# Optimization experiments

Hardware: AMD Instinct MI355X
Metric: run time of the kernel (lower is better)

The kernel has to match this reference:

```python
import jax, jax.numpy as jnp
import numpy as np

N_NODES = 100000
EPS = 1e-12  # F.normalize eps


def mean_aggregate(x, src, dst):
    # gather source features along edges, segment-mean into destinations
    msg = x[src]                                              # [E, D]
    summed = jax.ops.segment_sum(msg, dst, num_segments=N_NODES)  # [N, D]
    cnt = jax.ops.segment_sum(jnp.ones_like(dst, dtype=x.dtype), dst,
                              num_segments=N_NODES)           # [N]
    return summed / jnp.maximum(cnt, 1.0)[:, None]


def sage_conv(x, src, dst, W_l, b_l, W_r, normalize):
    agg = mean_aggregate(x, src, dst)
    out = agg @ W_l.T + b_l + x @ W_r.T  # lin_l(mean neigh) + lin_r(root)
    if normalize:
        norm = jnp.sqrt(jnp.sum(out * out, axis=-1, keepdims=True))
        out = out / jnp.maximum(norm, EPS)
    return out


def setup_inputs() -> dict:
    key = jax.random.key(0)
    ks = jax.random.split(key, 8)
    H, O = 128, 128
    s = 1.0 / np.sqrt(H)
    x = jax.random.normal(ks[0], (N_NODES, H), dtype=jnp.float32)
    edge_index = jax.random.randint(ks[1], (2, 1600000), 0, N_NODES, dtype=jnp.int64)
    return {
        "x": x,
        "edge_index": edge_index,
        "W1l": jax.random.uniform(ks[2], (H, H), jnp.float32, -s, s),
        "b1": jax.random.uniform(ks[3], (H,), jnp.float32, -s, s),
        "W1r": jax.random.uniform(ks[4], (H, H), jnp.float32, -s, s),
        "W2l": jax.random.uniform(ks[5], (O, H), jnp.float32, -s, s),
        "b2": jax.random.uniform(ks[6], (O,), jnp.float32, -s, s),
        "W2r": jax.random.uniform(ks[7], (O, H), jnp.float32, -s, s),
    }


def reference(x, edge_index, W1l, b1, W1r, W2l, b2, W2r):
    src, dst = edge_index[0], edge_index[1]
    h = sage_conv(x, src, dst, W1l, b1, W1r, normalize=True)
    h = jax.nn.relu(h)
    out = sage_conv(h, src, dst, W2l, b2, W2r, normalize=False)
    return out
```

## Files before the change

kernel.cpp:

```cpp
#include <hip/hip_runtime.h>
#include <hip/hip_bf16.h>
#include <hip/hip_fp16.h>

#define N_NODES 100000
#define DFEAT 128
#define SLAB 4096
#define BSHIFT 9
#define NBUCK 196

#define WS_CNT      0
#define WS_W16      100000
#define WS_BCNT     180000
#define WS_BBASE    180200
#define WS_BCUR     180400
#define WS_OFFS     200000
#define WS_ESRC     300608
#define WS_AGGH     1900608
#define WS_CASTH    8300608

typedef _Float16 half8 __attribute__((ext_vector_type(8)));
typedef _Float16 half2v __attribute__((ext_vector_type(2)));
typedef float floatx4 __attribute__((ext_vector_type(4)));

__global__ __launch_bounds__(256) void cast_x_kernel(const float* __restrict__ x,
                                                     __half* __restrict__ xh, int total4) {
    int stride = gridDim.x * 256;
    for (int i = blockIdx.x * 256 + threadIdx.x; i < total4; i += stride) {
        float4 v = ((const float4*)x)[i];
        __half2 h01 = __floats2half2_rn(v.x, v.y);
        __half2 h23 = __floats2half2_rn(v.z, v.w);
        uint2 o;
        o.x = *(unsigned int*)&h01;
        o.y = *(unsigned int*)&h23;
        ((uint2*)xh)[i] = o;
    }
}

__global__ __launch_bounds__(256) void cast_w_kernel(const float* __restrict__ W1l,
                                                     const float* __restrict__ W1r,
                                                     const float* __restrict__ W2l,
                                                     const float* __restrict__ W2r,
                                                     __half* __restrict__ w16) {
    int i = blockIdx.x * 256 + threadIdx.x;
    int m = i >> 12;
    int off = i & 4095;
    const float* Wp = (m == 0) ? W1l : (m == 1) ? W1r : (m == 2) ? W2l : W2r;
    float4 v = ((const float4*)Wp)[off];
    __half2 h01 = __floats2half2_rn(v.x, v.y);
    __half2 h23 = __floats2half2_rn(v.z, v.w);
    uint2 o;
    o.x = *(unsigned int*)&h01;
    o.y = *(unsigned int*)&h23;
    ((uint2*)w16)[i] = o;
}

__global__ __launch_bounds__(1024) void hist_kernel(const int* __restrict__ dst,
                                                    int* __restrict__ bcnt, int E) {
    __shared__ int lh[NBUCK];
    int t = threadIdx.x;
    if (t < NBUCK) lh[t] = 0;
    __syncthreads();
    int s0 = blockIdx.x * SLAB, s1 = min(E, s0 + SLAB);
    for (int i = s0 + t; i < s1; i += 1024)
        atomicAdd(&lh[dst[i] >> BSHIFT], 1);
    __syncthreads();
    if (t < NBUCK && lh[t] > 0) atomicAdd(&bcnt[t], lh[t]);
}

__global__ void bscan_kernel(const int* __restrict__ bcnt, int* __restrict__ bbase,
                             int* __restrict__ bcur, int E) {
    __shared__ int s[256];
    int t = threadIdx.x;
    int v = (t < NBUCK) ? bcnt[t] : 0;
    s[t] = v;
    __syncthreads();
    for (int d = 1; d < 256; d <<= 1) {
        int u = (t >= d) ? s[t - d] : 0;
        __syncthreads();
        s[t] += u;
        __syncthreads();
    }
    if (t < NBUCK) {
        int excl = s[t] - v;
        bbase[t] = excl;
        bcur[t] = excl;
    }
    if (t == 0) bbase[NBUCK] = E;
}

__global__ __launch_bounds__(512) void phase2_kernel(const int* __restrict__ src,
                                                     const int* __restrict__ dst,
                                                     int* __restrict__ bcur,
                                                     int* __restrict__ pairs,
                                                     int E) {
    __shared__ int lbase[NBUCK];
    __shared__ int lcur[NBUCK];
    __shared__ int lgb[NBUCK];
    __shared__ int sc[256];
    __shared__ int2 lp[SLAB];
    int b = blockIdx.x;
    int t = threadIdx.x;
    if (t < NBUCK) lbase[t] = 0;
    __syncthreads();
    int s0 = b * SLAB, s1 = min(E, s0 + SLAB);
    for (int i = s0 + t; i < s1; i += 512)
        atomicAdd(&lbase[dst[i] >> BSHIFT], 1);
    __syncthreads();
    int v = (t < NBUCK) ? lbase[t] : 0;
    if (t < 256) sc[t] = v;
    __syncthreads();
    for (int d = 1; d < 256; d <<= 1) {
        int u = (t >= d && t < 256) ? sc[t - d] : 0;
        __syncthreads();
        if (t < 256) sc[t] += u;
        __syncthreads();
    }
    if (t < NBUCK) {
        int excl = sc[t] - v;
        lbase[t] = excl;
        lcur[t] = excl;
        lgb[t] = (v > 0) ? atomicAdd(&bcur[t], v) : 0;
    }
    __syncthreads();
    for (int i = s0 + t; i < s1; i += 512) {
        int d = dst[i];
        int s = src[i];
        int bk = d >> BSHIFT;
        int pos = atomicAdd(&lcur[bk], 1);
        lp[pos] = make_int2(s, d);
    }
    __syncthreads();
    int m = s1 - s0;
    for (int i = t; i < m; i += 512) {
        int2 p = lp[i];
        int bk = p.y >> BSHIFT;
        pairs[lgb[bk] + (i - lbase[bk])] = ((p.y & 511) << 17) | p.x;
    }
}

__global__ __launch_bounds__(1024) void phase3_kernel(const int* __restrict__ pairs,
                                                      const int* __restrict__ bbase,
                                                      int* __restrict__ cnt,
                                                      int* __restrict__ offs,
                                                      int* __restrict__ esrc,
                                                      int n) {
    __shared__ int lcnt[512];
    __shared__ int sc[512];
    __shared__ int lexcl[512];
    int g = blockIdx.x;
    int node0 = g << BSHIFT;
    int t = threadIdx.x;
    if (t < 512) lcnt[t] = 0;
    __syncthreads();
    int S = bbase[g];
    int Eg = bbase[g + 1];
    for (int i = S + t; i < Eg; i += 1024)
        atomicAdd(&lcnt[pairs[i] >> 17], 1);
    __syncthreads();
    int v = (t < 512) ? lcnt[t] : 0;
    if (t < 512) sc[t] = v;
    __syncthreads();
    for (int d = 1; d < 512; d <<= 1) {
        int u = (t >= d && t < 512) ? sc[t - d] : 0;
        __syncthreads();
        if (t < 512) sc[t] += u;
        __syncthreads();
    }
    if (t < 512) {
        int excl = sc[t] - v;
        lexcl[t] = excl;
        int nd = node0 + t;
        if (nd < n) {
            cnt[nd] = v;
            offs[nd] = S + excl;
        }
    }
    __syncthreads();
    for (int i = S + t; i < Eg; i += 1024) {
        int p = pairs[i];
        int pos = atomicAdd(&lexcl[p >> 17], 1);
        esrc[S + pos] = p & 0x1FFFF;
    }
}

#define ACC(c, r)                        \
    s[c][0] += *(half2v*)&(r).x;         \
    s[c][1] += *(half2v*)&(r).y;         \
    s[c][2] += *(half2v*)&(r).z;         \
    s[c][3] += *(half2v*)&(r).w;

__global__ void aggregate_kernel(const __half* __restrict__ feat, const int* __restrict__ esrc,
                                 const int* __restrict__ offs, const int* __restrict__ cnt,
                                 __half* __restrict__ agg, int n) {
    int wid = (blockIdx.x * blockDim.x + threadIdx.x) >> 6;
    int lane = threadIdx.x & 63;
    int grp = lane >> 4;
    int l15 = lane & 15;
    int node = wid * 4 + grp;
    if (node >= n) return;
    int beg = offs[node];
    int deg = cnt[node];
    const _Float16* fbase = (const _Float16*)feat + l15 * 8;
    const int* ep = esrc + beg;

    half2v s[4][4];
#pragma unroll
    for (int c = 0; c < 4; c++)
#pragma unroll
        for (int k = 0; k < 4; k++) s[c][k] = (half2v)(_Float16)0;

    int j = 0;
    for (; j + 8 <= deg; j += 8) {
        int i0 = ep[j + 0], i1 = ep[j + 1], i2 = ep[j + 2], i3 = ep[j + 3];
        int i4 = ep[j + 4], i5 = ep[j + 5], i6 = ep[j + 6], i7 = ep[j + 7];
        uint4 r0 = *(const uint4*)(fbase + (size_t)i0 * DFEAT);
        uint4 r1 = *(const uint4*)(fbase + (size_t)i1 * DFEAT);
        uint4 r2 = *(const uint4*)(fbase + (size_t)i2 * DFEAT);
        uint4 r3 = *(const uint4*)(fbase + (size_t)i3 * DFEAT);
        uint4 r4 = *(const uint4*)(fbase + (size_t)i4 * DFEAT);
        uint4 r5 = *(const uint4*)(fbase + (size_t)i5 * DFEAT);
        uint4 r6 = *(const uint4*)(fbase + (size_t)i6 * DFEAT);
        uint4 r7 = *(const uint4*)(fbase + (size_t)i7 * DFEAT);
        ACC(0, r0) ACC(1, r1) ACC(2, r2) ACC(3, r3)
        ACC(0, r4) ACC(1, r5) ACC(2, r6) ACC(3, r7)
    }
    for (; j + 4 <= deg; j += 4) {
        int i0 = ep[j + 0], i1 = ep[j + 1], i2 = ep[j + 2], i3 = ep[j + 3];
        uint4 r0 = *(const uint4*)(fbase + (size_t)i0 * DFEAT);
        uint4 r1 = *(const uint4*)(fbase + (size_t)i1 * DFEAT);
        uint4 r2 = *(const uint4*)(fbase + (size_t)i2 * DFEAT);
        uint4 r3 = *(const uint4*)(fbase + (size_t)i3 * DFEAT);
        ACC(0, r0) ACC(1, r1) ACC(2, r2) ACC(3, r3)
    }
    if (j < deg) {
        int rem = deg - j;
        int i0 = ep[j];
        int i1 = ep[j + (rem > 1 ? 1 : 0)];
        int i2 = ep[j + (rem > 2 ? 2 : 0)];
        uint4 r0 = *(const uint4*)(fbase + (size_t)i0 * DFEAT);
        uint4 r1 = *(const uint4*)(fbase + (size_t)i1 * DFEAT);
        uint4 r2 = *(const uint4*)(fbase + (size_t)i2 * DFEAT);
        if (rem < 2) { r1.x = 0u; r1.y = 0u; r1.z = 0u; r1.w = 0u; }
        if (rem < 3) { r2.x = 0u; r2.y = 0u; r2.z = 0u; r2.w = 0u; }
        ACC(0, r0) ACC(1, r1) ACC(2, r2)
    }

    float scale = 1.0f / fmaxf((float)deg, 1.0f);
    float a[8];
#pragma unroll
    for (int k = 0; k < 4; k++) {
        a[2 * k]     = ((float)s[0][k].x + (float)s[1][k].x) + ((float)s[2][k].x + (float)s[3][k].x);
        a[2 * k + 1] = ((float)s[0][k].y + (float)s[1][k].y) + ((float)s[2][k].y + (float)s[3][k].y);
    }
    __half2 h0 = __floats2half2_rn(a[0] * scale, a[1] * scale);
    __half2 h1 = __floats2half2_rn(a[2] * scale, a[3] * scale);
    __half2 h2 = __floats2half2_rn(a[4] * scale, a[5] * scale);
    __half2 h3 = __floats2half2_rn(a[6] * scale, a[7] * scale);
    uint4 o;
    o.x = *(unsigned int*)&h0;
    o.y = *(unsigned int*)&h1;
    o.z = *(unsigned int*)&h2;
    o.w = *(unsigned int*)&h3;
    *(uint4*)(agg + (size_t)node * DFEAT + l15 * 8) = o;
}

template <bool NORM_RELU>
__global__ __launch_bounds__(256) void gemm64_kernel(
    const __half* __restrict__ A1_, const __half* __restrict__ A2_,
    const __half* __restrict__ Wl16, const __half* __restrict__ Wr16,
    const float* __restrict__ bias, float* __restrict__ out32,
    __half* __restrict__ out16, int n) {
    __shared__ __align__(16) _Float16 lw[128 * 136];

    const _Float16* A1 = (const _Float16*)A1_;
    const _Float16* A2 = (const _Float16*)A2_;
    const _Float16* wl = (const _Float16*)Wl16;
    const _Float16* wr = (const _Float16*)Wr16;

    const int lane = threadIdx.x & 63;
    const int w = threadIdx.x >> 6;
    const int quad = lane >> 4;
    const int l15 = lane & 15;
    const int i0 = blockIdx.x * 64 + w * 16;
    int r = i0 + l15;
    if (r >= n) r = n - 1;
    const int kq = quad * 8;

    half8 bf[4];
#pragma unroll
    for (int k = 0; k < 4; k++)
        bf[k] = *(const half8*)(A1 + (size_t)r * DFEAT + k * 32 + kq);

    {
        int t = threadIdx.x;
        int row = t >> 1;
        int cb = (t & 1) * 64;
        const uint4* sp = (const uint4*)(wl + row * DFEAT + cb);
        uint4* dp = (uint4*)&lw[row * 136 + cb];
#pragma unroll
        for (int q = 0; q < 8; q++) dp[q] = sp[q];
    }
    __syncthreads();

    floatx4 acc[8];
#pragma unroll
    for (int ft = 0; ft < 8; ft++) acc[ft] = (floatx4){0.f, 0.f, 0.f, 0.f};

#pragma unroll
    for (int kci = 0; kci < 4; kci++) {
#pragma unroll
        for (int ft = 0; ft < 8; ft++) {
            half8 a = *(const half8*)&lw[(ft * 16 + l15) * 136 + kci * 32 + kq];
            acc[ft] = __builtin_amdgcn_mfma_f32_16x16x32_f16(a, bf[kci], acc[ft], 0, 0, 0);
        }
    }

    half8 xf[4];
#pragma unroll
    for (int k = 0; k < 4; k++)
        xf[k] = *(const half8*)(A2 + (size_t)r * DFEAT + k * 32 + kq);

    __syncthreads();
    {
        int t = threadIdx.x;
        int row = t >> 1;
        int cb = (t & 1) * 64;
        const uint4* sp = (const uint4*)(wr + row * DFEAT + cb);
        uint4* dp = (uint4*)&lw[row * 136 + cb];
#pragma unroll
        for (int q = 0; q < 8; q++) dp[q] = sp[q];
    }
    __syncthreads();

#pragma unroll
    for (int kci = 0; kci < 4; kci++) {
#pragma unroll
        for (int ft = 0; ft < 8; ft++) {
            half8 a = *(const half8*)&lw[(ft * 16 + l15) * 136 + kci * 32 + kq];
            acc[ft] = __builtin_amdgcn_mfma_f32_16x16x32_f16(a, xf[kci], acc[ft], 0, 0, 0);
        }
    }

    int node = i0 + l15;
    float v[8][4];
#pragma unroll
    for (int ft = 0; ft < 8; ft++) {
        const float4 bq = *(const float4*)(bias + ft * 16 + quad * 4);
        v[ft][0] = acc[ft][0] + bq.x;
        v[ft][1] = acc[ft][1] + bq.y;
        v[ft][2] = acc[ft][2] + bq.z;
        v[ft][3] = acc[ft][3] + bq.w;
    }
    if (NORM_RELU) {
        float ss = 0.f;
#pragma unroll
        for (int ft = 0; ft < 8; ft++)
#pragma unroll
            for (int q = 0; q < 4; q++) ss = fmaf(v[ft][q], v[ft][q], ss);
        ss += __shfl_xor(ss, 16);
        ss += __shfl_xor(ss, 32);
        float inv = 1.0f / fmaxf(sqrtf(ss), 1e-12f);
#pragma unroll
        for (int ft = 0; ft < 8; ft++)
#pragma unroll
            for (int q = 0; q < 4; q++) v[ft][q] = fmaxf(v[ft][q] * inv, 0.0f);
    }
    if (node < n) {
        if (NORM_RELU) {
            __half* op = (__half*)out16 + (size_t)node * DFEAT + quad * 4;
#pragma unroll
            for (int ft = 0; ft < 8; ft++) {
                __half2 h01 = __floats2half2_rn(v[ft][0], v[ft][1]);
                __half2 h23 = __floats2half2_rn(v[ft][2], v[ft][3]);
                uint2 o;
                o.x = *(unsigned int*)&h01;
                o.y = *(unsigned int*)&h23;
                *(uint2*)(op + ft * 16) = o;
            }
        } else {
            float* op = out32 + (size_t)node * DFEAT + quad * 4;
#pragma unroll
            for (int ft = 0; ft < 8; ft++)
                *(float4*)(op + ft * 16) = make_float4(v[ft][0], v[ft][1], v[ft][2], v[ft][3]);
        }
    }
}

extern "C" void kernel_launch(void* const* d_in, const int* in_sizes, int n_in,
                              void* d_out, int out_size, void* d_ws, size_t ws_size,
                              hipStream_t stream) {
    const float* x = (const float*)d_in[0];
    const int* edge_index = (const int*)d_in[1];
    const float* W1l = (const float*)d_in[2];
    const float* b1 = (const float*)d_in[3];
    const float* W1r = (const float*)d_in[4];
    const float* W2l = (const float*)d_in[5];
    const float* b2 = (const float*)d_in[6];
    const float* W2r = (const float*)d_in[7];
    float* out = (float*)d_out;

    const int E = in_sizes[1] / 2;
    const int n = in_sizes[0] / DFEAT;

    int* ws = (int*)d_ws;
    int* cnt = ws + WS_CNT;
    __half* w16 = (__half*)(ws + WS_W16);
    int* bcnt = ws + WS_BCNT;
    int* bbase = ws + WS_BBASE;
    int* bcur = ws + WS_BCUR;
    int* offs = ws + WS_OFFS;
    int* esrc = ws + WS_ESRC;
    int* pairs = ws + WS_AGGH;
    __half* aggh = (__half*)(ws + WS_AGGH);
    __half* casth = (__half*)(ws + WS_CASTH);

    const int* src = edge_index;
    const int* dst = edge_index + E;

    const int bpart = (E + SLAB - 1) / SLAB;
    const int total4 = n * DFEAT / 4;

    __half* w1l16 = w16;
    __half* w1r16 = w16 + 16384;
    __half* w2l16 = w16 + 32768;
    __half* w2r16 = w16 + 49152;

    hipMemsetAsync(bcnt, 0, NBUCK * sizeof(int), stream);

    cast_x_kernel<<<2048, 256, 0, stream>>>(x, casth, total4);
    cast_w_kernel<<<64, 256, 0, stream>>>(W1l, W1r, W2l, W2r, w16);
    hist_kernel<<<bpart, 1024, 0, stream>>>(dst, bcnt, E);
    bscan_kernel<<<1, 256, 0, stream>>>(bcnt, bbase, bcur, E);
    phase2_kernel<<<bpart, 512, 0, stream>>>(src, dst, bcur, pairs, E);
    phase3_kernel<<<NBUCK, 1024, 0, stream>>>(pairs, bbase, cnt, offs, esrc, n);

    const int nwaves = (n + 3) / 4;
    const int aggb = (nwaves * 64 + 255) / 256;
    const int gemmb = (n + 63) / 64;

    aggregate_kernel<<<aggb, 256, 0, stream>>>(casth, esrc, offs, cnt, aggh, n);
    gemm64_kernel<true><<<gemmb, 256, 0, stream>>>(aggh, casth, w1l16, w1r16, b1,
                                                   nullptr, aggh, n);

    aggregate_kernel<<<aggb, 256, 0, stream>>>(aggh, esrc, offs, cnt, casth, n);
    gemm64_kernel<false><<<gemmb, 256, 0, stream>>>(casth, aggh, w2l16, w2r16, b2,
                                                    out, nullptr, n);
}
```

Before: 329.7 us.

## Make GEMM persistent with both weights resident in swizzled LDS; merge cast kernels

The per-tile GEMM kernel, which reloaded both weight matrices into LDS for every 64-row tile, is replaced by a persistent kernel with a fixed grid. Each block loads W_l and W_r once into 64 KB of XOR-swizzled LDS and loops over tiles, interleaving the two MFMA chains. The two cast kernels are merged into one launch. This trades weight-load and sync overhead for lower occupancy from the larger LDS footprint and a fixed grid size, and the layer-1 GEMM still writes into aggh while reading it, now across tiles within a block.

```diff
diff --git a/kernel.cpp b/kernel.cpp
--- a/kernel.cpp
+++ b/kernel.cpp
@@ -22,36 +22,36 @@
 typedef _Float16 half2v __attribute__((ext_vector_type(2)));
 typedef float floatx4 __attribute__((ext_vector_type(4)));
 
-__global__ __launch_bounds__(256) void cast_x_kernel(const float* __restrict__ x,
-                                                     __half* __restrict__ xh, int total4) {
+__global__ __launch_bounds__(256) void cast_kernel(const float* __restrict__ x,
+                                                   __half* __restrict__ xh, int total4,
+                                                   const float* __restrict__ W1l,
+                                                   const float* __restrict__ W1r,
+                                                   const float* __restrict__ W2l,
+                                                   const float* __restrict__ W2r,
+                                                   __half* __restrict__ w16) {
     int stride = gridDim.x * 256;
-    for (int i = blockIdx.x * 256 + threadIdx.x; i < total4; i += stride) {
-        float4 v = ((const float4*)x)[i];
+    int totalAll = total4 + 16384;
+    for (int i = blockIdx.x * 256 + threadIdx.x; i < totalAll; i += stride) {
+        float4 v;
+        uint2* dp;
+        if (i < total4) {
+            v = ((const float4*)x)[i];
+            dp = (uint2*)xh + i;
+        } else {
+            int j = i - total4;
+            int m = j >> 12;
+            int off = j & 4095;
+            const float* Wp = (m == 0) ? W1l : (m == 1) ? W1r : (m == 2) ? W2l : W2r;
+            v = ((const float4*)Wp)[off];
+            dp = (uint2*)w16 + j;
+        }
         __half2 h01 = __floats2half2_rn(v.x, v.y);
         __half2 h23 = __floats2half2_rn(v.z, v.w);
         uint2 o;
         o.x = *(unsigned int*)&h01;
         o.y = *(unsigned int*)&h23;
-        ((uint2*)xh)[i] = o;
-    }
-}
-
-__global__ __launch_bounds__(256) void cast_w_kernel(const float* __restrict__ W1l,
-                                                     const float* __restrict__ W1r,
-                                                     const float* __restrict__ W2l,
-                                                     const float* __restrict__ W2r,
-                                                     __half* __restrict__ w16) {
-    int i = blockIdx.x * 256 + threadIdx.x;
-    int m = i >> 12;
-    int off = i & 4095;
-    const float* Wp = (m == 0) ? W1l : (m == 1) ? W1r : (m == 2) ? W2l : W2r;
-    float4 v = ((const float4*)Wp)[off];
-    __half2 h01 = __floats2half2_rn(v.x, v.y);
-    __half2 h23 = __floats2half2_rn(v.z, v.w);
-    uint2 o;
-    o.x = *(unsigned int*)&h01;
-    o.y = *(unsigned int*)&h23;
-    ((uint2*)w16)[i] = o;
+        *dp = o;
+    }
 }
 
 __global__ __launch_bounds__(1024) void hist_kernel(const int* __restrict__ dst,
@@ -264,124 +264,118 @@
     *(uint4*)(agg + (size_t)node * DFEAT + l15 * 8) = o;
 }
 
+__device__ __forceinline__ int swz(int row, int bytecol) {
+    return row * 256 + (bytecol ^ ((row & 7) << 4));
+}
+
 template <bool NORM_RELU>
-__global__ __launch_bounds__(256) void gemm64_kernel(
+__global__ __launch_bounds__(256) void gemm_persist_kernel(
     const __half* __restrict__ A1_, const __half* __restrict__ A2_,
     const __half* __restrict__ Wl16, const __half* __restrict__ Wr16,
     const float* __restrict__ bias, float* __restrict__ out32,
-    __half* __restrict__ out16, int n) {
-    __shared__ __align__(16) _Float16 lw[128 * 136];
+    __half* __restrict__ out16, int n, int ntiles) {
+    extern __shared__ __align__(16) char lds[];
+    char* lwl = lds;
+    char* lwr = lds + 32768;
 
     const _Float16* A1 = (const _Float16*)A1_;
     const _Float16* A2 = (const _Float16*)A2_;
-    const _Float16* wl = (const _Float16*)Wl16;
-    const _Float16* wr = (const _Float16*)Wr16;
+    const char* wl = (const char*)Wl16;
+    const char* wr = (const char*)Wr16;
 
     const int lane = threadIdx.x & 63;
     const int w = threadIdx.x >> 6;
     const int quad = lane >> 4;
     const int l15 = lane & 15;
-    const int i0 = blockIdx.x * 64 + w * 16;
-    int r = i0 + l15;
-    if (r >= n) r = n - 1;
     const int kq = quad * 8;
-
-    half8 bf[4];
-#pragma unroll
-    for (int k = 0; k < 4; k++)
-        bf[k] = *(const half8*)(A1 + (size_t)r * DFEAT + k * 32 + kq);
 
     {
         int t = threadIdx.x;
         int row = t >> 1;
-        int cb = (t & 1) * 64;
-        const uint4* sp = (const uint4*)(wl + row * DFEAT + cb);
-        uint4* dp = (uint4*)&lw[row * 136 + cb];
-#pragma unroll
-        for (int q = 0; q < 8; q++) dp[q] = sp[q];
-    }
-    __syncthreads();
-
-    floatx4 acc[8];
-#pragma unroll
-    for (int ft = 0; ft < 8; ft++) acc[ft] = (floatx4){0.f, 0.f, 0.f, 0.f};
-
-#pragma unroll
-    for (int kci = 0; kci < 4; kci++) {
+        int cb = (t & 1) * 128;
+#pragma unroll
+        for (int q = 0; q < 8; q++) {
+            int bc = cb + q * 16;
+            int so = row * 256 + bc;
+            int off = swz(row, bc);
+            *(uint4*)(lwl + off) = *(const uint4*)(wl + so);
+            *(uint4*)(lwr + off) = *(const uint4*)(wr + so);
+        }
+    }
+    __syncthreads();
+
+    for (int tile = blockIdx.x; tile < ntiles; tile += gridDim.x) {
+        const int i0 = tile * 64 + w * 16;
+        int r = i0 + l15;
+        if (r >= n) r = n - 1;
+
+        half8 bf[4], xf[4];
+#pragma unroll
+        for (int k = 0; k < 4; k++) {
+            bf[k] = *(const half8*)(A1 + (size_t)r * DFEAT + k * 32 + kq);
+            xf[k] = *(const half8*)(A2 + (size_t)r * DFEAT + k * 32 + kq);
+        }
+
+        floatx4 acc[8];
+#pragma unroll
+        for (int ft = 0; ft < 8; ft++) acc[ft] = (floatx4){0.f, 0.f, 0.f, 0.f};
+
+#pragma unroll
+        for (int kci = 0; kci < 4; kci++) {
+            const int bc = kci * 64 + quad * 16;
+#pragma unroll
+            for (int ft = 0; ft < 8; ft++) {
+                int row = ft * 16 + l15;
+                int off = swz(row, bc);
+                half8 al = *(const half8*)(lwl + off);
+                half8 ar = *(const half8*)(lwr + off);
+                acc[ft] = __builtin_amdgcn_mfma_f32_16x16x32_f16(al, bf[kci], acc[ft], 0, 0, 0);
+                acc[ft] = __builtin_amdgcn_mfma_f32_16x16x32_f16(ar, xf[kci], acc[ft], 0, 0, 0);
+            }
+        }
+
+        int node = i0 + l15;
+        float v[8][4];
 #pragma unroll
         for (int ft = 0; ft < 8; ft++) {
-            half8 a = *(const half8*)&lw[(ft * 16 + l15) * 136 + kci * 32 + kq];
-            acc[ft] = __builtin_amdgcn_mfma_f32_16x16x32_f16(a, bf[kci], acc[ft], 0, 0, 0);
-        }
-    }
-
-    half8 xf[4];
-#pragma unroll
-    for (int k = 0; k < 4; k++)
-        xf[k] = *(const half8*)(A2 + (size_t)r * DFEAT + k * 32 + kq);
-
-    __syncthreads();
-    {
-        int t = threadIdx.x;
-        int row = t >> 1;
-        int cb = (t & 1) * 64;
-        const uint4* sp = (const uint4*)(wr + row * DFEAT + cb);
-        uint4* dp = (uint4*)&lw[row * 136 + cb];
-#pragma unroll
-        for (int q = 0; q < 8; q++) dp[q] = sp[q];
-    }
-    __syncthreads();
-
-#pragma unroll
-    for (int kci = 0; kci < 4; kci++) {
-#pragma unroll
-        for (int ft = 0; ft < 8; ft++) {
-            half8 a = *(const half8*)&lw[(ft * 16 + l15) * 136 + kci * 32 + kq];
-            acc[ft] = __builtin_amdgcn_mfma_f32_16x16x32_f16(a, xf[kci], acc[ft], 0, 0, 0);
-        }
-    }
-
-    int node = i0 + l15;
-    float v[8][4];
-#pragma unroll
-    for (int ft = 0; ft < 8; ft++) {
-        const float4 bq = *(const float4*)(bias + ft * 16 + quad * 4);
-        v[ft][0] = acc[ft][0] + bq.x;
-        v[ft][1] = acc[ft][1] + bq.y;
-        v[ft][2] = acc[ft][2] + bq.z;
-        v[ft][3] = acc[ft][3] + bq.w;
-    }
-    if (NORM_RELU) {
-        float ss = 0.f;
-#pragma unroll
-        for (int ft = 0; ft < 8; ft++)
-#pragma unroll
-            for (int q = 0; q < 4; q++) ss = fmaf(v[ft][q], v[ft][q], ss);
-        ss += __shfl_xor(ss, 16);
-        ss += __shfl_xor(ss, 32);
-        float inv = 1.0f / fmaxf(sqrtf(ss), 1e-12f);
-#pragma unroll
-        for (int ft = 0; ft < 8; ft++)
-#pragma unroll
-            for (int q = 0; q < 4; q++) v[ft][q] = fmaxf(v[ft][q] * inv, 0.0f);
-    }
-    if (node < n) {
+            const float4 bq = *(const float4*)(bias + ft * 16 + quad * 4);
+            v[ft][0] = acc[ft][0] + bq.x;
+            v[ft][1] = acc[ft][1] + bq.y;
+            v[ft][2] = acc[ft][2] + bq.z;
+            v[ft][3] = acc[ft][3] + bq.w;
+        }
         if (NORM_RELU) {
-            __half* op = (__half*)out16 + (size_t)node * DFEAT + quad * 4;
-#pragma unroll
-            for (int ft = 0; ft < 8; ft++) {
-                __half2 h01 = __floats2half2_rn(v[ft][0], v[ft][1]);
-                __half2 h23 = __floats2half2_rn(v[ft][2], v[ft][3]);
-                uint2 o;
-                o.x = *(unsigned int*)&h01;
-                o.y = *(unsigned int*)&h23;
-                *(uint2*)(op + ft * 16) = o;
+            float ss = 0.f;
+#pragma unroll
+            for (int ft = 0; ft < 8; ft++)
+#pragma unroll
+                for (int q = 0; q < 4; q++) ss = fmaf(v[ft][q], v[ft][q], ss);
+            ss += __shfl_xor(ss, 16);
+            ss += __shfl_xor(ss, 32);
+            float inv = 1.0f / fmaxf(sqrtf(ss), 1e-12f);
+#pragma unroll
+            for (int ft = 0; ft < 8; ft++)
+#pragma unroll
+                for (int q = 0; q < 4; q++) v[ft][q] = fmaxf(v[ft][q] * inv, 0.0f);
+        }
+        if (node < n) {
+            if (NORM_RELU) {
+                __half* op = (__half*)out16 + (size_t)node * DFEAT + quad * 4;
+#pragma unroll
+                for (int ft = 0; ft < 8; ft++) {
+                    __half2 h01 = __floats2half2_rn(v[ft][0], v[ft][1]);
+                    __half2 h23 = __floats2half2_rn(v[ft][2], v[ft][3]);
+                    uint2 o;
+                    o.x = *(unsigned int*)&h01;
+                    o.y = *(unsigned int*)&h23;
+                    *(uint2*)(op + ft * 16) = o;
+                }
+            } else {
+                float* op = out32 + (size_t)node * DFEAT + quad * 4;
+#pragma unroll
+                for (int ft = 0; ft < 8; ft++)
+                    *(float4*)(op + ft * 16) = make_float4(v[ft][0], v[ft][1], v[ft][2], v[ft][3]);
             }
-        } else {
-            float* op = out32 + (size_t)node * DFEAT + quad * 4;
-#pragma unroll
-            for (int ft = 0; ft < 8; ft++)
-                *(float4*)(op + ft * 16) = make_float4(v[ft][0], v[ft][1], v[ft][2], v[ft][3]);
         }
     }
 }
@@ -427,8 +421,7 @@
 
     hipMemsetAsync(bcnt, 0, NBUCK * sizeof(int), stream);
 
-    cast_x_kernel<<<2048, 256, 0, stream>>>(x, casth, total4);
-    cast_w_kernel<<<64, 256, 0, stream>>>(W1l, W1r, W2l, W2r, w16);
+    cast_kernel<<<2048, 256, 0, stream>>>(x, casth, total4, W1l, W1r, W2l, W2r, w16);
     hist_kernel<<<bpart, 1024, 0, stream>>>(dst, bcnt, E);
     bscan_kernel<<<1, 256, 0, stream>>>(bcnt, bbase, bcur, E);
     phase2_kernel<<<bpart, 512, 0, stream>>>(src, dst, bcur, pairs, E);
@@ -436,13 +429,14 @@
 
     const int nwaves = (n + 3) / 4;
     const int aggb = (nwaves * 64 + 255) / 256;
-    const int gemmb = (n + 63) / 64;
+    const int ntiles = (n + 63) / 64;
+    const int gemmb = 512;
 
     aggregate_kernel<<<aggb, 256, 0, stream>>>(casth, esrc, offs, cnt, aggh, n);
-    gemm64_kernel<true><<<gemmb, 256, 0, stream>>>(aggh, casth, w1l16, w1r16, b1,
-                                                   nullptr, aggh, n);
+    gemm_persist_kernel<true><<<gemmb, 256, 65536, stream>>>(
+        aggh, casth, w1l16, w1r16, b1, nullptr, aggh, n, ntiles);
 
     aggregate_kernel<<<aggb, 256, 0, stream>>>(aggh, esrc, offs, cnt, casth, n);
-    gemm64_kernel<false><<<gemmb, 256, 0, stream>>>(casth, aggh, w2l16, w2r16, b2,
-                                                    out, nullptr, n);
-}
+    gemm_persist_kernel<false><<<gemmb, 256, 65536, stream>>>(
+        casth, aggh, w2l16, w2r16, b2, out, nullptr, n, ntiles);
+}
```

Result: no change. 336.0 us (+1.9%).

## Fuse casts and memset, fold bucket scan into histogram, halve bucket size

Applied to the files above, without the earlier changes.

Merges the x and weight casts and the bucket-counter zeroing into one kernel. The bucket prefix scan moves into the last-finishing histogram block through a global completion counter, so one kernel launch and one memset go away. Buckets shrink to 256 nodes (391 buckets), which gives phase3 more blocks with less work each but enlarges the shared scans in phase2. The last-block pattern relies on threadfence and atomic ordering being correct.

```diff
diff --git a/kernel.cpp b/kernel.cpp
--- a/kernel.cpp
+++ b/kernel.cpp
@@ -5,14 +5,14 @@
 #define N_NODES 100000
 #define DFEAT 128
 #define SLAB 4096
-#define BSHIFT 9
-#define NBUCK 196
+#define BSHIFT 8
+#define NBUCK 391
 
 #define WS_CNT      0
 #define WS_W16      100000
 #define WS_BCNT     180000
-#define WS_BBASE    180200
-#define WS_BCUR     180400
+#define WS_BBASE    180400
+#define WS_BCUR     180800
 #define WS_OFFS     200000
 #define WS_ESRC     300608
 #define WS_AGGH     1900608
@@ -22,41 +22,49 @@
 typedef _Float16 half2v __attribute__((ext_vector_type(2)));
 typedef float floatx4 __attribute__((ext_vector_type(4)));
 
-__global__ __launch_bounds__(256) void cast_x_kernel(const float* __restrict__ x,
-                                                     __half* __restrict__ xh, int total4) {
+__global__ __launch_bounds__(256) void cast_kernel(const float* __restrict__ x,
+                                                   __half* __restrict__ xh, int total4,
+                                                   const float* __restrict__ W1l,
+                                                   const float* __restrict__ W1r,
+                                                   const float* __restrict__ W2l,
+                                                   const float* __restrict__ W2r,
+                                                   __half* __restrict__ w16,
+                                                   int* __restrict__ bcnt) {
+    int gtid = blockIdx.x * 256 + threadIdx.x;
+    if (gtid <= NBUCK) bcnt[gtid] = 0;
     int stride = gridDim.x * 256;
-    for (int i = blockIdx.x * 256 + threadIdx.x; i < total4; i += stride) {
-        float4 v = ((const float4*)x)[i];
+    int totalAll = total4 + 16384;
+    for (int i = gtid; i < totalAll; i += stride) {
+        float4 v;
+        uint2* dp;
+        if (i < total4) {
+            v = ((const float4*)x)[i];
+            dp = (uint2*)xh + i;
+        } else {
+            int j = i - total4;
+            int m = j >> 12;
+            int off = j & 4095;
+            const float* Wp = (m == 0) ? W1l : (m == 1) ? W1r : (m == 2) ? W2l : W2r;
+            v = ((const float4*)Wp)[off];
+            dp = (uint2*)w16 + j;
+        }
         __half2 h01 = __floats2half2_rn(v.x, v.y);
         __half2 h23 = __floats2half2_rn(v.z, v.w);
         uint2 o;
         o.x = *(unsigned int*)&h01;
         o.y = *(unsigned int*)&h23;
-        ((uint2*)xh)[i] = o;
-    }
-}
-
-__global__ __launch_bounds__(256) void cast_w_kernel(const float* __restrict__ W1l,
-                                                     const float* __restrict__ W1r,
-                                                     const float* __restrict__ W2l,
-                                                     const float* __restrict__ W2r,
-                                                     __half* __restrict__ w16) {
-    int i = blockIdx.x * 256 + threadIdx.x;
-    int m = i >> 12;
-    int off = i & 4095;
-    const float* Wp = (m == 0) ? W1l : (m == 1) ? W1r : (m == 2) ? W2l : W2r;
-    float4 v = ((const float4*)Wp)[off];
-    __half2 h01 = __floats2half2_rn(v.x, v.y);
-    __half2 h23 = __floats2half2_rn(v.z, v.w);
-    uint2 o;
-    o.x = *(unsigned int*)&h01;
-    o.y = *(unsigned int*)&h23;
-    ((uint2*)w16)[i] = o;
+        *dp = o;
+    }
 }
 
 __global__ __launch_bounds__(1024) void hist_kernel(const int* __restrict__ dst,
-                                                    int* __restrict__ bcnt, int E) {
+                                                    int* __restrict__ bcnt,
+                                                    int* __restrict__ bbase,
+                                                    int* __restrict__ bcur,
+                                                    int E, int nblocks) {
     __shared__ int lh[NBUCK];
+    __shared__ int sc[512];
+    __shared__ int lastFlag;
     int t = threadIdx.x;
     if (t < NBUCK) lh[t] = 0;
     __syncthreads();
@@ -65,27 +73,30 @@
         atomicAdd(&lh[dst[i] >> BSHIFT], 1);
     __syncthreads();
     if (t < NBUCK && lh[t] > 0) atomicAdd(&bcnt[t], lh[t]);
-}
-
-__global__ void bscan_kernel(const int* __restrict__ bcnt, int* __restrict__ bbase,
-                             int* __restrict__ bcur, int E) {
-    __shared__ int s[256];
-    int t = threadIdx.x;
-    int v = (t < NBUCK) ? bcnt[t] : 0;
-    s[t] = v;
-    __syncthreads();
-    for (int d = 1; d < 256; d <<= 1) {
-        int u = (t >= d) ? s[t - d] : 0;
+    if (t == 0) {
+        __threadfence();
+        int old = atomicAdd(&bcnt[NBUCK], 1);
+        lastFlag = (old == nblocks - 1) ? 1 : 0;
+    }
+    __syncthreads();
+    if (lastFlag) {
+        __threadfence();
+        int v = (t < NBUCK) ? bcnt[t] : 0;
+        if (t < 512) sc[t] = v;
         __syncthreads();
-        s[t] += u;
-        __syncthreads();
-    }
-    if (t < NBUCK) {
-        int excl = s[t] - v;
-        bbase[t] = excl;
-        bcur[t] = excl;
-    }
-    if (t == 0) bbase[NBUCK] = E;
+        for (int d = 1; d < 512; d <<= 1) {
+            int u = (t >= d && t < 512) ? sc[t - d] : 0;
+            __syncthreads();
+            if (t < 512) sc[t] += u;
+            __syncthreads();
+        }
+        if (t < NBUCK) {
+            int excl = sc[t] - v;
+            bbase[t] = excl;
+            bcur[t] = excl;
+        }
+        if (t == 0) bbase[NBUCK] = E;
+    }
 }
 
 __global__ __launch_bounds__(512) void phase2_kernel(const int* __restrict__ src,
@@ -96,7 +107,7 @@
     __shared__ int lbase[NBUCK];
     __shared__ int lcur[NBUCK];
     __shared__ int lgb[NBUCK];
-    __shared__ int sc[256];
+    __shared__ int sc[512];
     __shared__ int2 lp[SLAB];
     int b = blockIdx.x;
     int t = threadIdx.x;
@@ -107,12 +118,12 @@
         atomicAdd(&lbase[dst[i] >> BSHIFT], 1);
     __syncthreads();
     int v = (t < NBUCK) ? lbase[t] : 0;
-    if (t < 256) sc[t] = v;
-    __syncthreads();
-    for (int d = 1; d < 256; d <<= 1) {
-        int u = (t >= d && t < 256) ? sc[t - d] : 0;
+    sc[t] = v;
+    __syncthreads();
+    for (int d = 1; d < 512; d <<= 1) {
+        int u = (t >= d) ? sc[t - d] : 0;
         __syncthreads();
-        if (t < 256) sc[t] += u;
+        sc[t] += u;
         __syncthreads();
     }
     if (t < NBUCK) {
@@ -134,7 +145,7 @@
     for (int i = t; i < m; i += 512) {
         int2 p = lp[i];
         int bk = p.y >> BSHIFT;
-        pairs[lgb[bk] + (i - lbase[bk])] = ((p.y & 511) << 17) | p.x;
+        pairs[lgb[bk] + (i - lbase[bk])] = ((p.y & 255) << 17) | p.x;
     }
 }
 
@@ -144,29 +155,29 @@
                                                       int* __restrict__ offs,
                                                       int* __restrict__ esrc,
                                                       int n) {
-    __shared__ int lcnt[512];
-    __shared__ int sc[512];
-    __shared__ int lexcl[512];
+    __shared__ int lcnt[256];
+    __shared__ int sc[256];
+    __shared__ int lexcl[256];
     int g = blockIdx.x;
     int node0 = g << BSHIFT;
     int t = threadIdx.x;
-    if (t < 512) lcnt[t] = 0;
+    if (t < 256) lcnt[t] = 0;
     __syncthreads();
     int S = bbase[g];
     int Eg = bbase[g + 1];
     for (int i = S + t; i < Eg; i += 1024)
         atomicAdd(&lcnt[pairs[i] >> 17], 1);
     __syncthreads();
-    int v = (t < 512) ? lcnt[t] : 0;
-    if (t < 512) sc[t] = v;
-    __syncthreads();
-    for (int d = 1; d < 512; d <<= 1) {
-        int u = (t >= d && t < 512) ? sc[t - d] : 0;
+    int v = (t < 256) ? lcnt[t] : 0;
+    if (t < 256) sc[t] = v;
+    __syncthreads();
+    for (int d = 1; d < 256; d <<= 1) {
+        int u = (t >= d && t < 256) ? sc[t - d] : 0;
         __syncthreads();
-        if (t < 512) sc[t] += u;
+        if (t < 256) sc[t] += u;
         __syncthreads();
     }
-    if (t < 512) {
+    if (t < 256) {
         int excl = sc[t] - v;
         lexcl[t] = excl;
         int nd = node0 + t;
@@ -425,12 +436,8 @@
     __half* w2l16 = w16 + 32768;
     __half* w2r16 = w16 + 49152;
 
-    hipMemsetAsync(bcnt, 0, NBUCK * sizeof(int), stream);
-
-    cast_x_kernel<<<2048, 256, 0, stream>>>(x, casth, total4);
-    cast_w_kernel<<<64, 256, 0, stream>>>(W1l, W1r, W2l, W2r, w16);
-    hist_kernel<<<bpart, 1024, 0, stream>>>(dst, bcnt, E);
-    bscan_kernel<<<1, 256, 0, stream>>>(bcnt, bbase, bcur, E);
+    cast_kernel<<<2048, 256, 0, stream>>>(x, casth, total4, W1l, W1r, W2l, W2r, w16, bcnt);
+    hist_kernel<<<bpart, 1024, 0, stream>>>(dst, bcnt, bbase, bcur, E, bpart);
     phase2_kernel<<<bpart, 512, 0, stream>>>(src, dst, bcur, pairs, E);
     phase3_kernel<<<NBUCK, 1024, 0, stream>>>(pairs, bbase, cnt, offs, esrc, n);
 
```

Result: no change. 332.8 us (+0.9%).
